# Optimization experiments

Measured on AMD Instinct MI355X. Metric: run time of the kernel, lower is better.

## Reference

```python
import jax, jax.numpy as jnp
import numpy as np

N_NODES = 100000
N_EDGES = 1600000
N_FEAT = 64
HIDDEN = 16


def setup_inputs() -> dict:
    key = jax.random.key(0)
    ks = jax.random.split(key, 10)
    x = jax.random.normal(ks[0], (N_NODES, N_FEAT), dtype=jnp.float32)
    edge_index = jax.random.randint(ks[1], (2, N_EDGES), 0, N_NODES, dtype=jnp.int64)
    As = jax.random.normal(ks[2], (2, N_EDGES), dtype=jnp.float32)
    ws_weights = jax.random.normal(ks[3], (2,), dtype=jnp.float32)
    Wl1 = jax.random.normal(ks[4], (N_FEAT, HIDDEN), dtype=jnp.float32) / np.sqrt(N_FEAT)
    bl1 = jnp.zeros((HIDDEN,), dtype=jnp.float32)
    Wr1 = jax.random.normal(ks[5], (N_FEAT, HIDDEN), dtype=jnp.float32) / np.sqrt(N_FEAT)
    Wl2 = jax.random.normal(ks[6], (HIDDEN, 1), dtype=jnp.float32) / np.sqrt(HIDDEN)
    bl2 = jnp.zeros((1,), dtype=jnp.float32)
    Wr2 = jax.random.normal(ks[7], (HIDDEN, 1), dtype=jnp.float32) / np.sqrt(HIDDEN)
    return {"x": x, "edge_index": edge_index, "As": As, "ws_weights": ws_weights,
            "Wl1": Wl1, "bl1": bl1, "Wr1": Wr1, "Wl2": Wl2, "bl2": bl2, "Wr2": Wr2}


def reference(x, edge_index, As, ws_weights, Wl1, bl1, Wr1, Wl2, bl2, Wr2):
    # WeightedSumLayer: weighted sum of per-edge weight vectors
    ewm = jnp.einsum('m,me->e', ws_weights, As)  # [E]
    # edge mask (nonzero weighted sum keeps the edge); instead of slicing to a
    # data-dependent edge count, zero out masked messages (same aggregation).
    mask = (ewm != 0).astype(x.dtype)  # [E]
    src, dst = edge_index[0], edge_index[1]
    n = x.shape[0]

    # SAGEConv layer 1 (aggr='sum'): out = lin_l(sum_j x_j) + lin_r(x)
    msg1 = x[src] * mask[:, None]                             # [E, F]
    agg1 = jax.ops.segment_sum(msg1, dst, num_segments=n)     # [N, F]
    h = jax.nn.relu(agg1 @ Wl1 + bl1 + x @ Wr1)               # [N, H]

    # SAGEConv layer 2
    msg2 = h[src] * mask[:, None]                             # [E, H]
    agg2 = jax.ops.segment_sum(msg2, dst, num_segments=n)     # [N, H]
    out = agg2 @ Wl2 + bl2 + h @ Wr2                          # [N, 1]
    return out
```

## Files before the change

kernel.cpp:

```cpp
#include <hip/hip_runtime.h>
#include <hip/hip_bf16.h>

constexpr int NN = 100000;
constexpr int NE = 1600000;
constexpr int NF = 64;
constexpr int NH = 16;

constexpr int NPB  = 64;
constexpr int LB   = 6;
constexpr int NBKT = (NN + NPB - 1) / NPB;
constexpr int CAP  = 1280;
constexpr int CHUNK = 4096;
constexpr int NBLK_B = (NE + CHUNK - 1) / CHUNK;

__device__ __forceinline__ float bf16_to_f32(unsigned short u) {
    return __uint_as_float(((unsigned int)u) << 16);
}
__device__ __forceinline__ unsigned short f32_to_bf16(float f) {
    __hip_bfloat16 hb = __float2bfloat16(f);
    return *reinterpret_cast<unsigned short*>(&hb);
}

__global__ __launch_bounds__(256)
void k1_node_lin(const float* __restrict__ x,
                 const float* __restrict__ Wl1,
                 const float* __restrict__ Wr1,
                 unsigned short* __restrict__ p,
                 float* __restrict__ r)
{
    __shared__ float sW[2 * NF * NH];
    for (int i = threadIdx.x; i < NF * NH; i += 256) {
        sW[i]           = Wl1[i];
        sW[NF * NH + i] = Wr1[i];
    }
    __syncthreads();

    int n = blockIdx.x * 256 + threadIdx.x;
    if (n >= NN) return;

    float aL[NH], aR[NH];
#pragma unroll
    for (int j = 0; j < NH; ++j) { aL[j] = 0.f; aR[j] = 0.f; }

    const float4* xr = reinterpret_cast<const float4*>(x + (size_t)n * NF);
#pragma unroll
    for (int k4 = 0; k4 < NF / 4; ++k4) {
        float4 v = xr[k4];
        float xs[4] = {v.x, v.y, v.z, v.w};
#pragma unroll
        for (int t = 0; t < 4; ++t) {
            const float* wl = &sW[(k4 * 4 + t) * NH];
            const float* wr = &sW[NF * NH + (k4 * 4 + t) * NH];
#pragma unroll
            for (int j = 0; j < NH; ++j) {
                aL[j] = fmaf(xs[t], wl[j], aL[j]);
                aR[j] = fmaf(xs[t], wr[j], aR[j]);
            }
        }
    }

    unsigned int pu[8];
#pragma unroll
    for (int j2 = 0; j2 < 8; ++j2)
        pu[j2] = (unsigned int)f32_to_bf16(aL[2*j2]) |
                 ((unsigned int)f32_to_bf16(aL[2*j2+1]) << 16);
    uint4* pp = reinterpret_cast<uint4*>(p + (size_t)n * NH);
    pp[0] = make_uint4(pu[0], pu[1], pu[2], pu[3]);
    pp[1] = make_uint4(pu[4], pu[5], pu[6], pu[7]);

    float4* rp = reinterpret_cast<float4*>(r + (size_t)n * NH);
#pragma unroll
    for (int j4 = 0; j4 < NH / 4; ++j4)
        rp[j4] = make_float4(aR[j4*4], aR[j4*4+1], aR[j4*4+2], aR[j4*4+3]);
}

__global__ __launch_bounds__(256)
void k_bucket(const int* __restrict__ ei, const float* __restrict__ As,
              const float* __restrict__ ws,
              int* __restrict__ bcnt, unsigned int* __restrict__ bmem)
{
    __shared__ int lcnt[NBKT];
    __shared__ int lbase[NBKT];
    __shared__ unsigned int   sw[CHUNK];
    __shared__ unsigned short sbk[CHUNK];
    int tid = threadIdx.x;
    for (int i = tid; i < NBKT; i += 256) lcnt[i] = 0;
    __syncthreads();

    int base = blockIdx.x * CHUNK;
    float w0 = ws[0], w1 = ws[1];

#pragma unroll
    for (int j = 0; j < CHUNK / 256; ++j) {
        int idx = j * 256 + tid;
        int e = base + idx;
        unsigned int w = 0;
        unsigned short bk = 0xFFFFu;
        if (e < NE) {
            float ewm = w0 * As[e] + w1 * As[NE + e];
            if (ewm != 0.f) {
                int dst = ei[NE + e];
                bk = (unsigned short)(dst >> LB);
                w  = ((unsigned)ei[e] << LB) | (unsigned)(dst & (NPB - 1));
                atomicAdd(&lcnt[dst >> LB], 1);
            }
        }
        sw[idx]  = w;
        sbk[idx] = bk;
    }
    __syncthreads();

    for (int i = tid; i < NBKT; i += 256) {
        int c = lcnt[i];
        lbase[i] = c ? atomicAdd(&bcnt[i], c) : 0;
    }
    __syncthreads();
    for (int i = tid; i < NBKT; i += 256) lcnt[i] = 0;
    __syncthreads();

#pragma unroll
    for (int j = 0; j < CHUNK / 256; ++j) {
        int idx = j * 256 + tid;
        unsigned short bk = sbk[idx];
        if (bk != 0xFFFFu) {
            int rank = atomicAdd(&lcnt[bk], 1);
            int slot = lbase[bk] + rank;
            if (slot < CAP)
                bmem[(size_t)bk * CAP + slot] = sw[idx];
        }
    }
}

__global__ __launch_bounds__(256)
void k_agg1(const int* __restrict__ bcnt, unsigned int* __restrict__ bmem,
            const unsigned short* __restrict__ p, const float* __restrict__ r,
            const float* __restrict__ bl1, const float* __restrict__ Wl2,
            const float* __restrict__ bl2, const float* __restrict__ Wr2,
            float* __restrict__ q, float* __restrict__ out,
            int* __restrict__ gsoff)
{
    __shared__ unsigned int sbm[CAP];
    __shared__ unsigned int ssorted[CAP];
    __shared__ int hist[NPB];
    __shared__ int soff[NPB + 1];
    __shared__ int lrank[NPB];

    int b = blockIdx.x;
    int tid = threadIdx.x;
    if (tid < NPB) { hist[tid] = 0; lrank[tid] = 0; }
    __syncthreads();

    int cnt = min(bcnt[b], CAP);

    for (int i = tid; i < cnt; i += 256) {
        unsigned int w = bmem[(size_t)b * CAP + i];
        sbm[i] = w;
        atomicAdd(&hist[w & (NPB - 1)], 1);
    }
    __syncthreads();

    if (tid < NPB) {
        int v = hist[tid];
        int inc = v;
#pragma unroll
        for (int off = 1; off < NPB; off <<= 1) {
            int u = __shfl_up(inc, off);
            if (tid >= off) inc += u;
        }
        soff[tid + 1] = inc;
        if (tid == 0) soff[0] = 0;
    }
    __syncthreads();

    for (int i = tid; i < cnt; i += 256) {
        unsigned int w = sbm[i];
        int dl = w & (NPB - 1);
        int pos = soff[dl] + atomicAdd(&lrank[dl], 1);
        ssorted[pos] = w;
    }
    __syncthreads();

    for (int i = tid; i < cnt; i += 256)
        bmem[(size_t)b * CAP + i] = ssorted[i];
    if (tid < NPB + 1)
        gsoff[(size_t)b * (NPB + 1) + tid] = soff[tid];

    int g = tid >> 4, k = tid & 15;
    int n0 = b * NPB;
#pragma unroll
    for (int jj = 0; jj < 4; ++jj) {
        int nl = g * 4 + jj;
        int s = soff[nl], e = soff[nl + 1];
        float a = 0.f;
        int i = s;
        for (; i + 3 < e; i += 4) {
            unsigned w0 = ssorted[i], w1 = ssorted[i+1], w2 = ssorted[i+2], w3 = ssorted[i+3];
            float v0 = bf16_to_f32(p[(size_t)(w0 >> LB) * NH + k]);
            float v1 = bf16_to_f32(p[(size_t)(w1 >> LB) * NH + k]);
            float v2 = bf16_to_f32(p[(size_t)(w2 >> LB) * NH + k]);
            float v3 = bf16_to_f32(p[(size_t)(w3 >> LB) * NH + k]);
            a += (v0 + v1) + (v2 + v3);
        }
        for (; i < e; ++i)
            a += bf16_to_f32(p[(size_t)(ssorted[i] >> LB) * NH + k]);

        int n = n0 + nl;
        if (n < NN) {
            float h = a + r[(size_t)n * NH + k] + bl1[k];
            h = h > 0.f ? h : 0.f;
            float qv = h * Wl2[k];
            float sv = h * Wr2[k];
#pragma unroll
            for (int m = 8; m >= 1; m >>= 1) {
                qv += __shfl_xor(qv, m);
                sv += __shfl_xor(sv, m);
            }
            if (k == 0) {
                q[n]   = qv;
                out[n] = sv + bl2[0];
            }
        }
    }
}

__global__ __launch_bounds__(256)
void k_agg2(const int* __restrict__ gsoff, const unsigned int* __restrict__ bmem,
            const float* __restrict__ q, float* __restrict__ out)
{
    int n = blockIdx.x * 256 + threadIdx.x;
    if (n >= NN) return;
    int b  = n >> LB;
    int dl = n & (NPB - 1);
    int s = gsoff[(size_t)b * (NPB + 1) + dl];
    int e = gsoff[(size_t)b * (NPB + 1) + dl + 1];
    const unsigned int* bm = bmem + (size_t)b * CAP;

    float a = 0.f;
    int i = s;
    for (; i + 3 < e; i += 4) {
        unsigned w0 = bm[i], w1 = bm[i+1], w2 = bm[i+2], w3 = bm[i+3];
        a += (q[w0 >> LB] + q[w1 >> LB]) + (q[w2 >> LB] + q[w3 >> LB]);
    }
    for (; i < e; ++i)
        a += q[bm[i] >> LB];
    out[n] += a;
}

extern "C" void kernel_launch(void* const* d_in, const int* in_sizes, int n_in,
                              void* d_out, int out_size, void* d_ws, size_t ws_size,
                              hipStream_t stream)
{
    const float* x   = (const float*)d_in[0];
    const int*   ei  = (const int*)  d_in[1];
    const float* As  = (const float*)d_in[2];
    const float* ws  = (const float*)d_in[3];
    const float* Wl1 = (const float*)d_in[4];
    const float* bl1 = (const float*)d_in[5];
    const float* Wr1 = (const float*)d_in[6];
    const float* Wl2 = (const float*)d_in[7];
    const float* bl2 = (const float*)d_in[8];
    const float* Wr2 = (const float*)d_in[9];
    float* out = (float*)d_out;

    unsigned short* p     = (unsigned short*)d_ws;
    float*          r     = (float*)(p + (size_t)NN * NH);
    float*          q     = r + (size_t)NN * NH;
    int*            bcnt  = (int*)(q + NN);
    int*            gsoff = bcnt + NBKT;
    unsigned int*   bmem  = (unsigned int*)(gsoff + (size_t)NBKT * (NPB + 1));

    hipMemsetAsync(bcnt, 0, NBKT * sizeof(int), stream);

    k1_node_lin<<<(NN + 255) / 256, 256, 0, stream>>>(x, Wl1, Wr1, p, r);
    k_bucket<<<NBLK_B, 256, 0, stream>>>(ei, As, ws, bcnt, bmem);
    k_agg1<<<NBKT, 256, 0, stream>>>(bcnt, bmem, p, r, bl1, Wl2, bl2, Wr2, q, out, gsoff);
    k_agg2<<<(NN + 255) / 256, 256, 0, stream>>>(gsoff, bmem, q, out);
}
```

Measured before the change: 185.7 us.

## Enlarge dst buckets and capture atomic ranks in the first pass to skip recount

Buckets now hold 128 destination nodes instead of 64, and the bucketing kernel runs with bigger chunks and 512-thread blocks. Both the bucketing kernel and the per-bucket sort keep the rank returned by the first shared atomicAdd, so the second atomic pass and the counter reset are gone. The larger buckets cut the number of global bucket counters and blocks, which lowers contention on global atomics. In exchange, shared-memory use per block rises (lower occupancy), the prefix scan becomes a multi-barrier shared loop over 128 entries, and each thread aggregates 8 nodes instead of 4.

New measurement: 181.0 us. -2.5%, faster.

```diff
diff --git a/kernel.cpp b/kernel.cpp
--- a/kernel.cpp
+++ b/kernel.cpp
@@ -6,11 +6,12 @@
 constexpr int NF = 64;
 constexpr int NH = 16;
 
-constexpr int NPB  = 64;
-constexpr int LB   = 6;
+constexpr int NPB  = 128;
+constexpr int LB   = 7;
 constexpr int NBKT = (NN + NPB - 1) / NPB;
-constexpr int CAP  = 1280;
-constexpr int CHUNK = 4096;
+constexpr int CAP  = 2560;
+constexpr int CHUNK = 8192;
+constexpr int TB_B  = 512;
 constexpr int NBLK_B = (NE + CHUNK - 1) / CHUNK;
 
 __device__ __forceinline__ float bf16_to_f32(unsigned short u) {
@@ -74,56 +75,55 @@
         rp[j4] = make_float4(aR[j4*4], aR[j4*4+1], aR[j4*4+2], aR[j4*4+3]);
 }
 
-__global__ __launch_bounds__(256)
+__global__ __launch_bounds__(TB_B)
 void k_bucket(const int* __restrict__ ei, const float* __restrict__ As,
               const float* __restrict__ ws,
               int* __restrict__ bcnt, unsigned int* __restrict__ bmem)
 {
+    __shared__ unsigned int sw[CHUNK];
+    __shared__ unsigned int srk[CHUNK];
     __shared__ int lcnt[NBKT];
     __shared__ int lbase[NBKT];
-    __shared__ unsigned int   sw[CHUNK];
-    __shared__ unsigned short sbk[CHUNK];
     int tid = threadIdx.x;
-    for (int i = tid; i < NBKT; i += 256) lcnt[i] = 0;
+    for (int i = tid; i < NBKT; i += TB_B) lcnt[i] = 0;
     __syncthreads();
 
     int base = blockIdx.x * CHUNK;
     float w0 = ws[0], w1 = ws[1];
 
 #pragma unroll
-    for (int j = 0; j < CHUNK / 256; ++j) {
-        int idx = j * 256 + tid;
+    for (int j = 0; j < CHUNK / TB_B; ++j) {
+        int idx = j * TB_B + tid;
         int e = base + idx;
-        unsigned int w = 0;
-        unsigned short bk = 0xFFFFu;
+        unsigned int w = 0, rk = 0xFFFFFFFFu;
         if (e < NE) {
             float ewm = w0 * As[e] + w1 * As[NE + e];
             if (ewm != 0.f) {
                 int dst = ei[NE + e];
-                bk = (unsigned short)(dst >> LB);
+                int bk  = dst >> LB;
                 w  = ((unsigned)ei[e] << LB) | (unsigned)(dst & (NPB - 1));
-                atomicAdd(&lcnt[dst >> LB], 1);
+                int rank = atomicAdd(&lcnt[bk], 1);
+                rk = ((unsigned)bk << 13) | (unsigned)rank;
             }
         }
         sw[idx]  = w;
-        sbk[idx] = bk;
-    }
-    __syncthreads();
-
-    for (int i = tid; i < NBKT; i += 256) {
+        srk[idx] = rk;
+    }
+    __syncthreads();
+
+    for (int i = tid; i < NBKT; i += TB_B) {
         int c = lcnt[i];
         lbase[i] = c ? atomicAdd(&bcnt[i], c) : 0;
     }
     __syncthreads();
-    for (int i = tid; i < NBKT; i += 256) lcnt[i] = 0;
-    __syncthreads();
-
-#pragma unroll
-    for (int j = 0; j < CHUNK / 256; ++j) {
-        int idx = j * 256 + tid;
-        unsigned short bk = sbk[idx];
-        if (bk != 0xFFFFu) {
-            int rank = atomicAdd(&lcnt[bk], 1);
+
+#pragma unroll
+    for (int j = 0; j < CHUNK / TB_B; ++j) {
+        int idx = j * TB_B + tid;
+        unsigned int rk = srk[idx];
+        if (rk != 0xFFFFFFFFu) {
+            int bk   = rk >> 13;
+            int rank = rk & 0x1FFF;
             int slot = lbase[bk] + rank;
             if (slot < CAP)
                 bmem[(size_t)bk * CAP + slot] = sw[idx];
@@ -142,41 +142,47 @@
     __shared__ unsigned int sbm[CAP];
     __shared__ unsigned int ssorted[CAP];
     __shared__ int hist[NPB];
+    __shared__ int scan[NPB];
     __shared__ int soff[NPB + 1];
-    __shared__ int lrank[NPB];
 
     int b = blockIdx.x;
     int tid = threadIdx.x;
-    if (tid < NPB) { hist[tid] = 0; lrank[tid] = 0; }
+    if (tid < NPB) hist[tid] = 0;
     __syncthreads();
 
     int cnt = min(bcnt[b], CAP);
 
-    for (int i = tid; i < cnt; i += 256) {
-        unsigned int w = bmem[(size_t)b * CAP + i];
-        sbm[i] = w;
-        atomicAdd(&hist[w & (NPB - 1)], 1);
-    }
-    __syncthreads();
-
-    if (tid < NPB) {
-        int v = hist[tid];
-        int inc = v;
-#pragma unroll
-        for (int off = 1; off < NPB; off <<= 1) {
-            int u = __shfl_up(inc, off);
-            if (tid >= off) inc += u;
-        }
-        soff[tid + 1] = inc;
-        if (tid == 0) soff[0] = 0;
-    }
-    __syncthreads();
-
-    for (int i = tid; i < cnt; i += 256) {
-        unsigned int w = sbm[i];
-        int dl = w & (NPB - 1);
-        int pos = soff[dl] + atomicAdd(&lrank[dl], 1);
-        ssorted[pos] = w;
+    int rk[CAP / 256];
+#pragma unroll
+    for (int j = 0; j < CAP / 256; ++j) {
+        int i = j * 256 + tid;
+        if (i < cnt) {
+            unsigned int w = bmem[(size_t)b * CAP + i];
+            sbm[i] = w;
+            rk[j] = atomicAdd(&hist[w & (NPB - 1)], 1);
+        }
+    }
+    __syncthreads();
+
+    if (tid < NPB) scan[tid] = hist[tid];
+    __syncthreads();
+    for (int off = 1; off < NPB; off <<= 1) {
+        int u = (tid < NPB && tid >= off) ? scan[tid - off] : 0;
+        __syncthreads();
+        if (tid < NPB) scan[tid] += u;
+        __syncthreads();
+    }
+    if (tid < NPB) soff[tid + 1] = scan[tid];
+    if (tid == 0) soff[0] = 0;
+    __syncthreads();
+
+#pragma unroll
+    for (int j = 0; j < CAP / 256; ++j) {
+        int i = j * 256 + tid;
+        if (i < cnt) {
+            unsigned int w = sbm[i];
+            ssorted[soff[w & (NPB - 1)] + rk[j]] = w;
+        }
     }
     __syncthreads();
 
@@ -188,8 +194,8 @@
     int g = tid >> 4, k = tid & 15;
     int n0 = b * NPB;
 #pragma unroll
-    for (int jj = 0; jj < 4; ++jj) {
-        int nl = g * 4 + jj;
+    for (int jj = 0; jj < 8; ++jj) {
+        int nl = g * 8 + jj;
         int s = soff[nl], e = soff[nl + 1];
         float a = 0.f;
         int i = s;
@@ -272,7 +278,7 @@
     hipMemsetAsync(bcnt, 0, NBKT * sizeof(int), stream);
 
     k1_node_lin<<<(NN + 255) / 256, 256, 0, stream>>>(x, Wl1, Wr1, p, r);
-    k_bucket<<<NBLK_B, 256, 0, stream>>>(ei, As, ws, bcnt, bmem);
+    k_bucket<<<NBLK_B, TB_B, 0, stream>>>(ei, As, ws, bcnt, bmem);
     k_agg1<<<NBKT, 256, 0, stream>>>(bcnt, bmem, p, r, bl1, Wl2, bl2, Wr2, q, out, gsoff);
     k_agg2<<<(NN + 255) / 256, 256, 0, stream>>>(gsoff, bmem, q, out);
 }
```
